# Performance work log

Hardware: AMD Instinct MI355X
Metric: run time of the kernel (lower is better)

Reference implementation:

```python
import jax, jax.numpy as jnp
import numpy as np

NUM_PROPS = 512
D = 2 * NUM_PROPS          # n_embd
NUM_STEPS = 32
LN_EPS = 1e-5
_SQRT_2_OVER_PI = float(np.sqrt(2.0 / np.pi))


def gelu_new(x):
    # GPT-2 'gelu_new' tanh approximation
    return 0.5 * x * (1.0 + jnp.tanh(_SQRT_2_OVER_PI * (x + 0.044715 * x ** 3)))


def layernorm(x, g, b):
    mu = jnp.mean(x, axis=-1, keepdims=True)
    var = jnp.mean((x - mu) ** 2, axis=-1, keepdims=True)
    return (x - mu) * jax.lax.rsqrt(var + LN_EPS) * g + b


def setup_inputs() -> dict:
    key = jax.random.key(0)
    ks = jax.random.split(key, 16)
    s = 0.02
    inp = {
        "tokens": jax.random.randint(ks[0], (16, 256, D), 0, 2, dtype=jnp.int64),
        # GPT2 block params (Conv1D convention: weight [in, out])
        "W_qkv": jax.random.normal(ks[1], (D, 3 * D), jnp.float32) * s,
        "b_qkv": jnp.zeros((3 * D,), jnp.float32),
        "W_aproj": jax.random.normal(ks[2], (D, D), jnp.float32) * s,
        "b_aproj": jnp.zeros((D,), jnp.float32),
        "g_ln1": jnp.ones((D,), jnp.float32),
        "b_ln1": jnp.zeros((D,), jnp.float32),
        "g_ln2": jnp.ones((D,), jnp.float32),
        "b_ln2": jnp.zeros((D,), jnp.float32),
        "W_fc": jax.random.normal(ks[3], (D, 4 * D), jnp.float32) * s,
        "b_fc": jnp.zeros((4 * D,), jnp.float32),
        "W_mproj": jax.random.normal(ks[4], (4 * D, D), jnp.float32) * s,
        "b_mproj": jnp.zeros((D,), jnp.float32),
        "g_lnf": jnp.ones((D,), jnp.float32),
        "b_lnf": jnp.zeros((D,), jnp.float32),
        # classification head: nn.Linear(d, num_labels, bias=False), weight [num_labels, d]
        "W_score": jax.random.normal(ks[5], (NUM_PROPS, D), jnp.float32) * s,
    }
    return inp


def gpt2_logits(x, W_qkv, b_qkv, W_aproj, b_aproj, g_ln1, b_ln1, g_ln2, b_ln2,
                W_fc, b_fc, W_mproj, b_mproj, g_lnf, b_lnf, W_score):
    # x: [B, S, D] float embeddings (wpe is zeroed in the original module)
    S = x.shape[1]
    h = layernorm(x, g_ln1, b_ln1)
    qkv = h @ W_qkv + b_qkv
    q, k, v = jnp.split(qkv, 3, axis=-1)  # single head, head_dim = D
    scores = jnp.einsum("bqd,bkd->bqk", q, k) / jnp.sqrt(jnp.float32(D))
    causal = jnp.tril(jnp.ones((S, S), dtype=bool))
    scores = jnp.where(causal, scores, jnp.finfo(scores.dtype).min)
    attn = jax.nn.softmax(scores, axis=-1)
    x = x + jnp.einsum("bqk,bkd->bqd", attn, v) @ W_aproj + b_aproj
    h2 = layernorm(x, g_ln2, b_ln2)
    x = x + gelu_new(h2 @ W_fc + b_fc) @ W_mproj + b_mproj
    x = layernorm(x, g_lnf, b_lnf)
    # sequence classification: logits of the LAST token (inputs_embeds path)
    return x[:, -1, :] @ W_score.T  # [B, num_props]


def reference(tokens, W_qkv, b_qkv, W_aproj, b_aproj, g_ln1, b_ln1, g_ln2, b_ln2,
              W_fc, b_fc, W_mproj, b_mproj, g_lnf, b_lnf, W_score):
    all_toks = tokens.astype(jnp.float32)  # [B, L, D]
    logits_per_step = []
    for _ in range(NUM_STEPS):  # full recompute each step, no KV cache (faithful)
        logits = gpt2_logits(all_toks, W_qkv, b_qkv, W_aproj, b_aproj,
                             g_ln1, b_ln1, g_ln2, b_ln2, W_fc, b_fc,
                             W_mproj, b_mproj, g_lnf, b_lnf, W_score)
        succ = (logits > 0).astype(jnp.float32)  # hard threshold (non-diff, as .long())
        succ_tok = jnp.concatenate([jnp.zeros_like(succ), succ], axis=-1)[:, None, :]
        all_toks = jnp.concatenate([all_toks, jax.lax.stop_gradient(succ_tok)], axis=1)
        logits_per_step.append(logits)
    return jnp.stack(logits_per_step, axis=1)  # [B, num_steps, num_props]
```

## Files before the change

### kernel.cpp

```cpp
#include <hip/hip_runtime.h>
#include <math.h>

#ifndef M_PI
#define M_PI 3.14159265358979323846
#endif

#define BD 256
#define NB 16
#define DIM 1024
#define SMAX 288
#define NSTEPS 32
#define NPROPS 512
#define NTOK (16 * 256 * 1024)

__device__ __forceinline__ double wred_sum(double v) {
#pragma unroll
    for (int o = 32; o > 0; o >>= 1) v += __shfl_down(v, o, 64);
    return v;
}
__device__ __forceinline__ double wred_max(double v) {
#pragma unroll
    for (int o = 32; o > 0; o >>= 1) { double w = __shfl_down(v, o, 64); if (w > v) v = w; }
    return v;
}
__device__ double block_sum(double v, double* sc) {
    v = wred_sum(v);
    int tid = threadIdx.x;
    if ((tid & 63) == 0) sc[tid >> 6] = v;
    __syncthreads();
    double r = sc[0] + sc[1] + sc[2] + sc[3];
    __syncthreads();
    return r;
}
__device__ double block_max(double v, double* sc) {
    v = wred_max(v);
    int tid = threadIdx.x;
    if ((tid & 63) == 0) sc[tid >> 6] = v;
    __syncthreads();
    double r = fmax(fmax(sc[0], sc[1]), fmax(sc[2], sc[3]));
    __syncthreads();
    return r;
}

__global__ __launch_bounds__(256) void k_tok_convert(const int* __restrict__ tok32,
                                                     signed char* __restrict__ tokc) {
    __shared__ int flag;
    int tid = threadIdx.x;
    if (tid == 0) {
        int nz = 0;
        for (int i = 1; i < 512; i += 2) nz |= tok32[i];
        flag = nz;
    }
    __syncthreads();
    bool is64 = (flag == 0);
#pragma unroll
    for (int it = 0; it < 4; ++it) {
        size_t idx = (size_t)blockIdx.x * 1024 + it * BD + tid;
        int v = is64 ? tok32[2 * idx] : tok32[idx];
        tokc[idx] = (signed char)v;
    }
}

__global__ __launch_bounds__(256) void k_prefix_stats(const signed char* __restrict__ tokc,
                                                      double* __restrict__ mu, double* __restrict__ rs) {
    __shared__ double sc[4];
    int T = blockIdx.x, tid = threadIdx.x;
    const signed char* row = tokc + (size_t)T * DIM;
    double s = 0;
    for (int i = tid; i < DIM; i += BD) s += (double)row[i];
    s = block_sum(s, sc);
    double m = s * (1.0 / 1024.0);
    double ss = 0;
    for (int i = tid; i < DIM; i += BD) { double d = (double)row[i] - m; ss += d * d; }
    ss = block_sum(ss, sc);
    if (tid == 0) { mu[T] = m; rs[T] = 1.0 / sqrt(ss * (1.0 / 1024.0) + 1e-5); }
}

__global__ __launch_bounds__(256) void k_init(const signed char* __restrict__ tokc,
                                              const double* __restrict__ mu, const double* __restrict__ rs,
                                              double* __restrict__ xl,
                                              double* __restrict__ mub, double* __restrict__ rsb) {
    int b = blockIdx.x, tid = threadIdx.x;
    int T = b * 256 + 255;
    if (tid == 0) { mub[b] = mu[T]; rsb[b] = rs[T]; }
    for (int i = tid; i < DIM; i += BD)
        xl[b * DIM + i] = (double)tokc[(size_t)T * DIM + i];
}

__global__ __launch_bounds__(256) void k_prefix(const signed char* __restrict__ tokc,
        const double* __restrict__ mu, const double* __restrict__ rs,
        const float* __restrict__ Wqkv, const float* __restrict__ bqkv,
        const float* __restrict__ g1, const float* __restrict__ b1,
        float* __restrict__ Kcf, float* __restrict__ Vcf) {
    __shared__ float Hs[64 * 65];
    __shared__ float Ws[64 * 64];
    int tid = threadIdx.x;
    int tx = tid & 63, ty = tid >> 6;
    int j0 = blockIdx.x * 64;
    int T0 = blockIdx.y * 64;
    float acc[16];
#pragma unroll
    for (int a = 0; a < 16; ++a) acc[a] = 0.f;
    for (int kc = 0; kc < DIM; kc += 64) {
#pragma unroll
        for (int it = 0; it < 16; ++it) {
            int idx = tid + it * BD;
            int k = idx & 63, t = idx >> 6;
            int T = T0 + t;
            double x = (double)tokc[(size_t)T * DIM + kc + k];
            Hs[k * 65 + t] = (float)((x - mu[T]) * rs[T] * (double)g1[kc + k] + (double)b1[kc + k]);
        }
#pragma unroll
        for (int it = 0; it < 16; ++it) {
            int idx = tid + it * BD;
            int k = idx >> 6, j = idx & 63;
            Ws[k * 64 + j] = Wqkv[(size_t)(kc + k) * 3072 + 1024 + j0 + j];
        }
        __syncthreads();
#pragma unroll 4
        for (int k = 0; k < 64; ++k) {
            float w = Ws[k * 64 + tx];
#pragma unroll
            for (int a = 0; a < 16; ++a)
                acc[a] += Hs[k * 65 + ty * 16 + a] * w;
        }
        __syncthreads();
    }
    int colg = j0 + tx;
    float bias = bqkv[1024 + colg];
    bool isK = (colg < 1024);
#pragma unroll
    for (int a = 0; a < 16; ++a) {
        int T = T0 + ty * 16 + a;
        int b = T >> 8, pos = T & 255;
        float v = acc[a] + bias;
        if (isK) Kcf[((size_t)b * SMAX + pos) * DIM + colg] = v;
        else     Vcf[((size_t)b * SMAX + pos) * DIM + colg - 1024] = v;
    }
}

__global__ __launch_bounds__(256) void k_qkv(const double* __restrict__ xl,
        const double* __restrict__ mub, const double* __restrict__ rsb,
        const float* __restrict__ g1, const float* __restrict__ b1,
        const float* __restrict__ Wqkv, float* __restrict__ P1) {
    __shared__ double As[16 * 64];
    __shared__ float  Ws[64 * 64];
    int tid = threadIdx.x, tx = tid & 63, ty = tid >> 6;
    int j0 = blockIdx.x * 64;
    int k0 = blockIdx.y * 128;
    double acc[4] = {0, 0, 0, 0};
    for (int kc = 0; kc < 128; kc += 64) {
#pragma unroll
        for (int it = 0; it < 4; ++it) {
            int idx = tid + it * BD;
            int b = idx >> 6, k = idx & 63;
            int kk = k0 + kc + k;
            As[b * 64 + k] = (xl[(size_t)b * DIM + kk] - mub[b]) * rsb[b] * (double)g1[kk] + (double)b1[kk];
        }
#pragma unroll
        for (int it = 0; it < 16; ++it) {
            int idx = tid + it * BD;
            int k = idx >> 6, j = idx & 63;
            Ws[k * 64 + j] = Wqkv[(size_t)(k0 + kc + k) * 3072 + j0 + j];
        }
        __syncthreads();
#pragma unroll 8
        for (int k = 0; k < 64; ++k) {
            double w = (double)Ws[k * 64 + tx];
            acc[0] += As[(ty * 4 + 0) * 64 + k] * w;
            acc[1] += As[(ty * 4 + 1) * 64 + k] * w;
            acc[2] += As[(ty * 4 + 2) * 64 + k] * w;
            acc[3] += As[(ty * 4 + 3) * 64 + k] * w;
        }
        __syncthreads();
    }
#pragma unroll
    for (int a = 0; a < 4; ++a)
        P1[((size_t)(blockIdx.y * 16 + ty * 4 + a)) * 3072 + j0 + tx] = (float)acc[a];
}

__global__ __launch_bounds__(256) void mm16(const double* __restrict__ A, int K,
        const float* __restrict__ W, int ldw, double* __restrict__ P, int ncols) {
    __shared__ double As[16 * 64];
    __shared__ float  Ws[64 * 64];
    int tid = threadIdx.x, tx = tid & 63, ty = tid >> 6;
    int j0 = blockIdx.x * 64;
    int klen = K / gridDim.y;
    int k0 = blockIdx.y * klen;
    double acc[4] = {0, 0, 0, 0};
    for (int kc = 0; kc < klen; kc += 64) {
#pragma unroll
        for (int it = 0; it < 4; ++it) {
            int idx = tid + it * BD;
            int b = idx >> 6, k = idx & 63;
            As[b * 64 + k] = A[(size_t)b * K + k0 + kc + k];
        }
#pragma unroll
        for (int it = 0; it < 16; ++it) {
            int idx = tid + it * BD;
            int k = idx >> 6, j = idx & 63;
            Ws[k * 64 + j] = W[(size_t)(k0 + kc + k) * ldw + j0 + j];
        }
        __syncthreads();
#pragma unroll 8
        for (int k = 0; k < 64; ++k) {
            double w = (double)Ws[k * 64 + tx];
            acc[0] += As[(ty * 4 + 0) * 64 + k] * w;
            acc[1] += As[(ty * 4 + 1) * 64 + k] * w;
            acc[2] += As[(ty * 4 + 2) * 64 + k] * w;
            acc[3] += As[(ty * 4 + 3) * 64 + k] * w;
        }
        __syncthreads();
    }
#pragma unroll
    for (int a = 0; a < 4; ++a)
        P[((size_t)(blockIdx.y * 16 + ty * 4 + a)) * ncols + j0 + tx] = acc[a];
}

__global__ __launch_bounds__(256) void mm16f(const double* __restrict__ A, int K,
        const float* __restrict__ W, int ldw, float* __restrict__ P, int ncols) {
    __shared__ double As[16 * 64];
    __shared__ float  Ws[64 * 64];
    int tid = threadIdx.x, tx = tid & 63, ty = tid >> 6;
    int j0 = blockIdx.x * 64;
    int klen = K / gridDim.y;
    int k0 = blockIdx.y * klen;
    double acc[4] = {0, 0, 0, 0};
    for (int kc = 0; kc < klen; kc += 64) {
#pragma unroll
        for (int it = 0; it < 4; ++it) {
            int idx = tid + it * BD;
            int b = idx >> 6, k = idx & 63;
            As[b * 64 + k] = A[(size_t)b * K + k0 + kc + k];
        }
#pragma unroll
        for (int it = 0; it < 16; ++it) {
            int idx = tid + it * BD;
            int k = idx >> 6, j = idx & 63;
            Ws[k * 64 + j] = W[(size_t)(k0 + kc + k) * ldw + j0 + j];
        }
        __syncthreads();
#pragma unroll 8
        for (int k = 0; k < 64; ++k) {
            double w = (double)Ws[k * 64 + tx];
            acc[0] += As[(ty * 4 + 0) * 64 + k] * w;
            acc[1] += As[(ty * 4 + 1) * 64 + k] * w;
            acc[2] += As[(ty * 4 + 2) * 64 + k] * w;
            acc[3] += As[(ty * 4 + 3) * 64 + k] * w;
        }
        __syncthreads();
    }
#pragma unroll
    for (int a = 0; a < 4; ++a)
        P[((size_t)(blockIdx.y * 16 + ty * 4 + a)) * ncols + j0 + tx] = (float)acc[a];
}

__global__ __launch_bounds__(256) void mm16_t(const double* __restrict__ A, int K,
        const float* __restrict__ Wt, double* __restrict__ P, int ncols) {
    __shared__ double As[16 * 64];
    __shared__ float  Ws[64 * 65];
    int tid = threadIdx.x, tx = tid & 63, ty = tid >> 6;
    int j0 = blockIdx.x * 64;
    int klen = K / gridDim.y;
    int k0 = blockIdx.y * klen;
    double acc[4] = {0, 0, 0, 0};
    for (int kc = 0; kc < klen; kc += 64) {
#pragma unroll
        for (int it = 0; it < 4; ++it) {
            int idx = tid + it * BD;
            int b = idx >> 6, k = idx & 63;
            As[b * 64 + k] = A[(size_t)b * K + k0 + kc + k];
        }
#pragma unroll
        for (int it = 0; it < 16; ++it) {
            int idx = tid + it * BD;
            int j = idx >> 6, k = idx & 63;
            Ws[k * 65 + j] = Wt[(size_t)(j0 + j) * K + k0 + kc + k];
        }
        __syncthreads();
#pragma unroll 8
        for (int k = 0; k < 64; ++k) {
            double w = (double)Ws[k * 65 + tx];
            acc[0] += As[(ty * 4 + 0) * 64 + k] * w;
            acc[1] += As[(ty * 4 + 1) * 64 + k] * w;
            acc[2] += As[(ty * 4 + 2) * 64 + k] * w;
            acc[3] += As[(ty * 4 + 3) * 64 + k] * w;
        }
        __syncthreads();
    }
#pragma unroll
    for (int a = 0; a < 4; ++a)
        P[((size_t)(blockIdx.y * 16 + ty * 4 + a)) * ncols + j0 + tx] = acc[a];
}

__global__ __launch_bounds__(256) void k_scores(const float* __restrict__ P1,
        const float* __restrict__ bqkv, float* __restrict__ Kcf, float* __restrict__ Vcf,
        double* __restrict__ sco, int S) {
    __shared__ double qs[DIM];
    __shared__ float  ksf[DIM];
    int b = blockIdx.x, tid = threadIdx.x;
    int pos = S - 1;
    for (int col = tid; col < DIM; col += BD) {
        double s = (double)bqkv[col];
#pragma unroll
        for (int ks = 0; ks < 8; ++ks) s += (double)P1[((size_t)(ks * 16 + b)) * 3072 + col];
        qs[col] = s;
    }
    if ((int)blockIdx.y == (pos >> 5)) {
        for (int col = tid; col < DIM; col += BD) {
            double sk = (double)bqkv[1024 + col];
            double sv = (double)bqkv[2048 + col];
#pragma unroll
            for (int ks = 0; ks < 8; ++ks) {
                const float* Pr = &P1[((size_t)(ks * 16 + b)) * 3072];
                sk += (double)Pr[1024 + col];
                sv += (double)Pr[2048 + col];
            }
            float kf = (float)sk;
            ksf[col] = kf;
            Kcf[((size_t)b * SMAX + pos) * DIM + col] = kf;
            Vcf[((size_t)b * SMAX + pos) * DIM + col] = (float)sv;
        }
    }
    __syncthreads();
    int lane = tid & 63, w = tid >> 6;
    int base = blockIdx.y * 32 + w * 8;
    for (int r = 0; r < 8; ++r) {
        int p = base + r;
        if (p >= S) break;
        double acc = 0;
        const float4* kp4 = (p == pos) ? (const float4*)ksf
                                       : (const float4*)(Kcf + ((size_t)b * SMAX + p) * DIM);
#pragma unroll
        for (int ii = 0; ii < 4; ++ii) {
            float4 kv = kp4[lane + 64 * ii];
            int e = 4 * (lane + 64 * ii);
            acc += qs[e] * (double)kv.x + qs[e + 1] * (double)kv.y
                 + qs[e + 2] * (double)kv.z + qs[e + 3] * (double)kv.w;
        }
        acc = wred_sum(acc);
        if (lane == 0) sco[b * SMAX + p] = acc * 0.03125;
    }
}

__global__ __launch_bounds__(256) void k_attnp(const double* __restrict__ sco, const float* __restrict__ Vcf,
                                               double* __restrict__ AOp, int S) {
    __shared__ double ps[SMAX];
    __shared__ double sc[4];
    int b = blockIdx.x, sub = blockIdx.y, tid = threadIdx.x;
    int dch = sub & 3, sch = sub >> 2;
    double lm = -1e300;
    for (int i = tid; i < S; i += BD) { double v = sco[b * SMAX + i]; ps[i] = v; if (v > lm) lm = v; }
    __syncthreads();
    double mx = block_max(lm, sc);
    double le = 0;
    for (int i = tid; i < S; i += BD) { double e = exp(ps[i] - mx); ps[i] = e; le += e; }
    double den = block_sum(le, sc);
    int d = dch * 256 + tid;
    int p0 = sch * 36, p1 = p0 + 36; if (p1 > S) p1 = S;
    const float* Vb = Vcf + (size_t)b * SMAX * DIM + d;
    double a0 = 0, a1 = 0, a2 = 0, a3 = 0;
    int p = p0;
    for (; p + 4 <= p1; p += 4) {
        a0 += ps[p + 0] * (double)Vb[(size_t)(p + 0) * DIM];
        a1 += ps[p + 1] * (double)Vb[(size_t)(p + 1) * DIM];
        a2 += ps[p + 2] * (double)Vb[(size_t)(p + 2) * DIM];
        a3 += ps[p + 3] * (double)Vb[(size_t)(p + 3) * DIM];
    }
    for (; p < p1; ++p) a0 += ps[p] * (double)Vb[(size_t)p * DIM];
    AOp[((size_t)(sch * 16 + b)) * DIM + d] = ((a0 + a1) + (a2 + a3)) / den;
}

__global__ __launch_bounds__(256) void k_aproj(const double* __restrict__ AOp,
        const float* __restrict__ Wap, double* __restrict__ P2) {
    __shared__ double As[16 * 64];
    __shared__ float  Ws[64 * 64];
    int tid = threadIdx.x, tx = tid & 63, ty = tid >> 6;
    int j0 = blockIdx.x * 64;
    int k0 = blockIdx.y * 128;
    double acc[4] = {0, 0, 0, 0};
    for (int kc = 0; kc < 128; kc += 64) {
#pragma unroll
        for (int it = 0; it < 4; ++it) {
            int idx = tid + it * BD;
            int b = idx >> 6, k = idx & 63;
            const double* col = AOp + (size_t)b * DIM + k0 + kc + k;
            double s = 0;
#pragma unroll
            for (int sct = 0; sct < 8; ++sct) s += col[(size_t)sct * 16 * DIM];
            As[b * 64 + k] = s;
        }
#pragma unroll
        for (int it = 0; it < 16; ++it) {
            int idx = tid + it * BD;
            int k = idx >> 6, j = idx & 63;
            Ws[k * 64 + j] = Wap[(size_t)(k0 + kc + k) * DIM + j0 + j];
        }
        __syncthreads();
#pragma unroll 8
        for (int k = 0; k < 64; ++k) {
            double w = (double)Ws[k * 64 + tx];
            acc[0] += As[(ty * 4 + 0) * 64 + k] * w;
            acc[1] += As[(ty * 4 + 1) * 64 + k] * w;
            acc[2] += As[(ty * 4 + 2) * 64 + k] * w;
            acc[3] += As[(ty * 4 + 3) * 64 + k] * w;
        }
        __syncthreads();
    }
#pragma unroll
    for (int a = 0; a < 4; ++a)
        P2[((size_t)(blockIdx.y * 16 + ty * 4 + a)) * DIM + j0 + tx] = acc[a];
}

__global__ __launch_bounds__(256) void k_ln2(const double* __restrict__ xl, const double* __restrict__ P2,
        const float* __restrict__ bap, const float* __restrict__ g2, const float* __restrict__ b2,
        double* __restrict__ x2, double* __restrict__ h2) {
    __shared__ double xs[DIM];
    __shared__ double sc[4];
    int b = blockIdx.x, tid = threadIdx.x;
    for (int i = tid; i < DIM; i += BD) {
        double s = xl[b * DIM + i] + (double)bap[i];
        for (int ks = 0; ks < 8; ++ks) s += P2[((size_t)(ks * 16 + b)) * DIM + i];
        xs[i] = s; x2[b * DIM + i] = s;
    }
    __syncthreads();
    double s = 0;
    for (int i = tid; i < DIM; i += BD) s += xs[i];
    s = block_sum(s, sc);
    double m = s * (1.0 / 1024.0);
    double ss = 0;
    for (int i = tid; i < DIM; i += BD) { double d = xs[i] - m; ss += d * d; }
    ss = block_sum(ss, sc);
    double r = 1.0 / sqrt(ss * (1.0 / 1024.0) + 1e-5);
    for (int i = tid; i < DIM; i += BD)
        h2[b * DIM + i] = (xs[i] - m) * r * (double)g2[i] + (double)b2[i];
}

__global__ __launch_bounds__(256) void k_gelu(const float* __restrict__ P3, const float* __restrict__ bfc,
                                              double* __restrict__ m) {
    int b = blockIdx.x;
    int i = blockIdx.y * BD + threadIdx.x;
    double u = (double)bfc[i];
    for (int ks = 0; ks < 8; ++ks) u += (double)P3[((size_t)(ks * 16 + b)) * 4096 + i];
    double c = sqrt(2.0 / M_PI);
    double inner = c * (u + 0.044715 * u * u * u);
    m[(size_t)b * 4096 + i] = 0.5 * u * (1.0 + tanh(inner));
}

__global__ __launch_bounds__(256) void k_lnf(const double* __restrict__ x2, const double* __restrict__ P4,
        const float* __restrict__ bmp, const float* __restrict__ gf, const float* __restrict__ bf,
        double* __restrict__ hf) {
    __shared__ double xs[DIM];
    __shared__ double sc[4];
    int b = blockIdx.x, tid = threadIdx.x;
    for (int i = tid; i < DIM; i += BD) {
        double s = x2[b * DIM + i] + (double)bmp[i];
        for (int ks = 0; ks < 16; ++ks) s += P4[((size_t)(ks * 16 + b)) * DIM + i];
        xs[i] = s;
    }
    __syncthreads();
    double s = 0;
    for (int i = tid; i < DIM; i += BD) s += xs[i];
    s = block_sum(s, sc);
    double m = s * (1.0 / 1024.0);
    double ss = 0;
    for (int i = tid; i < DIM; i += BD) { double d = xs[i] - m; ss += d * d; }
    ss = block_sum(ss, sc);
    double r = 1.0 / sqrt(ss * (1.0 / 1024.0) + 1e-5);
    for (int i = tid; i < DIM; i += BD)
        hf[b * DIM + i] = (xs[i] - m) * r * (double)gf[i] + (double)bf[i];
}

__global__ __launch_bounds__(256) void k_final(const double* __restrict__ P5, float* __restrict__ out,
                                               double* __restrict__ xl,
                                               double* __restrict__ mub, double* __restrict__ rsb, int t) {
    __shared__ double sc[4];
    int b = blockIdx.x, tid = threadIdx.x;
    double cnt = 0;
    for (int p = tid; p < NPROPS; p += BD) {
        double lg = 0;
        for (int ks = 0; ks < 8; ++ks) lg += P5[((size_t)(ks * 16 + b)) * NPROPS + p];
        out[((size_t)b * NSTEPS + t) * NPROPS + p] = (float)lg;
        double bit = (lg > 0.0) ? 1.0 : 0.0;
        xl[b * DIM + p] = 0.0;
        xl[b * DIM + NPROPS + p] = bit;
        cnt += bit;
    }
    double s = block_sum(cnt, sc);
    double mean = s * (1.0 / 1024.0);
    double var = mean - mean * mean;
    double r = 1.0 / sqrt(var + 1e-5);
    if (tid == 0) { mub[b] = mean; rsb[b] = r; }
}

extern "C" void kernel_launch(void* const* d_in, const int* in_sizes, int n_in,
                              void* d_out, int out_size, void* d_ws, size_t ws_size,
                              hipStream_t stream) {
    const int*   tok  = (const int*)d_in[0];
    const float* Wqkv = (const float*)d_in[1];
    const float* bqkv = (const float*)d_in[2];
    const float* Wap  = (const float*)d_in[3];
    const float* bap  = (const float*)d_in[4];
    const float* g1   = (const float*)d_in[5];
    const float* b1   = (const float*)d_in[6];
    const float* g2   = (const float*)d_in[7];
    const float* b2   = (const float*)d_in[8];
    const float* Wfc  = (const float*)d_in[9];
    const float* bfc  = (const float*)d_in[10];
    const float* Wmp  = (const float*)d_in[11];
    const float* bmp  = (const float*)d_in[12];
    const float* gf   = (const float*)d_in[13];
    const float* bf   = (const float*)d_in[14];
    const float* Wsc  = (const float*)d_in[15];
    float* out = (float*)d_out;

    char* w = (char*)d_ws;
    size_t off = 0;
    auto alloc = [&](size_t bytes) -> void* {
        void* p = (void*)(w + off);
        off += (bytes + 255) & ~(size_t)255;
        return p;
    };
    float*       Kcf  = (float*)alloc((size_t)NB * SMAX * DIM * 4);
    float*       Vcf  = (float*)alloc((size_t)NB * SMAX * DIM * 4);
    double*      mu   = (double*)alloc(4096 * 8);
    double*      rs   = (double*)alloc(4096 * 8);
    double*      mub  = (double*)alloc(NB * 8);
    double*      rsb  = (double*)alloc(NB * 8);
    double*      xl   = (double*)alloc((size_t)NB * DIM * 8);
    double*      sco  = (double*)alloc((size_t)NB * SMAX * 8);
    double*      AOp  = (double*)alloc((size_t)8 * NB * DIM * 8);
    double*      x2   = (double*)alloc((size_t)NB * DIM * 8);
    double*      h2   = (double*)alloc((size_t)NB * DIM * 8);
    double*      m_   = (double*)alloc((size_t)NB * 4096 * 8);
    double*      hf   = (double*)alloc((size_t)NB * DIM * 8);
    float*       P1   = (float*)alloc((size_t)8 * NB * 3072 * 4);
    double*      P2   = (double*)alloc((size_t)8 * NB * 1024 * 8);
    float*       P3   = (float*)alloc((size_t)8 * NB * 4096 * 4);
    double*      P4   = (double*)alloc((size_t)16 * NB * 1024 * 8);
    double*      P5   = (double*)alloc((size_t)8 * NB * 512 * 8);
    signed char* tokc = (signed char*)alloc((size_t)NTOK);
    if (off > ws_size) return;

    k_tok_convert<<<4096, BD, 0, stream>>>(tok, tokc);
    k_prefix_stats<<<4096, BD, 0, stream>>>(tokc, mu, rs);
    k_init<<<NB, BD, 0, stream>>>(tokc, mu, rs, xl, mub, rsb);
    k_prefix<<<dim3(32, 64), BD, 0, stream>>>(tokc, mu, rs, Wqkv, bqkv, g1, b1, Kcf, Vcf);

    for (int t = 0; t < NSTEPS; ++t) {
        int S = 256 + t;
        k_qkv<<<dim3(48, 8), BD, 0, stream>>>(xl, mub, rsb, g1, b1, Wqkv, P1);
        k_scores<<<dim3(NB, 9), BD, 0, stream>>>(P1, bqkv, Kcf, Vcf, sco, S);
        k_attnp<<<dim3(NB, 32), BD, 0, stream>>>(sco, Vcf, AOp, S);
        k_aproj<<<dim3(16, 8), BD, 0, stream>>>(AOp, Wap, P2);
        k_ln2<<<NB, BD, 0, stream>>>(xl, P2, bap, g2, b2, x2, h2);
        mm16f<<<dim3(64, 8), BD, 0, stream>>>(h2, 1024, Wfc, 4096, P3, 4096);
        k_gelu<<<dim3(NB, 16), BD, 0, stream>>>(P3, bfc, m_);
        mm16<<<dim3(16, 16), BD, 0, stream>>>(m_, 4096, Wmp, 1024, P4, 1024);
        k_lnf<<<NB, BD, 0, stream>>>(x2, P4, bmp, gf, bf, hf);
        mm16_t<<<dim3(8, 8), BD, 0, stream>>>(hf, 1024, Wsc, P5, 512);
        k_final<<<NB, BD, 0, stream>>>(P5, out, xl, mub, rsb, t);
    }
}
```

Baseline: 3.593 ms.

## Store intermediate activations and partials in fp32, fuse token convert with stats

```diff
diff --git a/kernel.cpp b/kernel.cpp
--- a/kernel.cpp
+++ b/kernel.cpp
@@ -42,10 +42,12 @@
     return r;
 }
 
-__global__ __launch_bounds__(256) void k_tok_convert(const int* __restrict__ tok32,
-                                                     signed char* __restrict__ tokc) {
+__global__ __launch_bounds__(256) void k_tok_stats(const int* __restrict__ tok32,
+                                                   signed char* __restrict__ tokc,
+                                                   double* __restrict__ mu, double* __restrict__ rs) {
     __shared__ int flag;
-    int tid = threadIdx.x;
+    __shared__ double sc[4];
+    int T = blockIdx.x, tid = threadIdx.x;
     if (tid == 0) {
         int nz = 0;
         for (int i = 1; i < 512; i += 2) nz |= tok32[i];
@@ -53,24 +55,19 @@
     }
     __syncthreads();
     bool is64 = (flag == 0);
+    signed char* row = tokc + (size_t)T * DIM;
+    double s = 0;
 #pragma unroll
     for (int it = 0; it < 4; ++it) {
-        size_t idx = (size_t)blockIdx.x * 1024 + it * BD + tid;
+        size_t idx = (size_t)T * 1024 + it * BD + tid;
         int v = is64 ? tok32[2 * idx] : tok32[idx];
-        tokc[idx] = (signed char)v;
-    }
-}
-
-__global__ __launch_bounds__(256) void k_prefix_stats(const signed char* __restrict__ tokc,
-                                                      double* __restrict__ mu, double* __restrict__ rs) {
-    __shared__ double sc[4];
-    int T = blockIdx.x, tid = threadIdx.x;
-    const signed char* row = tokc + (size_t)T * DIM;
-    double s = 0;
-    for (int i = tid; i < DIM; i += BD) s += (double)row[i];
+        row[it * BD + tid] = (signed char)v;
+        s += (double)v;
+    }
     s = block_sum(s, sc);
     double m = s * (1.0 / 1024.0);
     double ss = 0;
+    __syncthreads();
     for (int i = tid; i < DIM; i += BD) { double d = (double)row[i] - m; ss += d * d; }
     ss = block_sum(ss, sc);
     if (tid == 0) { mu[T] = m; rs[T] = 1.0 / sqrt(ss * (1.0 / 1024.0) + 1e-5); }
@@ -78,13 +75,13 @@
 
 __global__ __launch_bounds__(256) void k_init(const signed char* __restrict__ tokc,
                                               const double* __restrict__ mu, const double* __restrict__ rs,
-                                              double* __restrict__ xl,
+                                              float* __restrict__ xl,
                                               double* __restrict__ mub, double* __restrict__ rsb) {
     int b = blockIdx.x, tid = threadIdx.x;
     int T = b * 256 + 255;
     if (tid == 0) { mub[b] = mu[T]; rsb[b] = rs[T]; }
     for (int i = tid; i < DIM; i += BD)
-        xl[b * DIM + i] = (double)tokc[(size_t)T * DIM + i];
+        xl[b * DIM + i] = (float)tokc[(size_t)T * DIM + i];
 }
 
 __global__ __launch_bounds__(256) void k_prefix(const signed char* __restrict__ tokc,
@@ -139,7 +136,7 @@
     }
 }
 
-__global__ __launch_bounds__(256) void k_qkv(const double* __restrict__ xl,
+__global__ __launch_bounds__(256) void k_qkv(const float* __restrict__ xl,
         const double* __restrict__ mub, const double* __restrict__ rsb,
         const float* __restrict__ g1, const float* __restrict__ b1,
         const float* __restrict__ Wqkv, float* __restrict__ P1) {
@@ -155,7 +152,7 @@
             int idx = tid + it * BD;
             int b = idx >> 6, k = idx & 63;
             int kk = k0 + kc + k;
-            As[b * 64 + k] = (xl[(size_t)b * DIM + kk] - mub[b]) * rsb[b] * (double)g1[kk] + (double)b1[kk];
+            As[b * 64 + k] = ((double)xl[(size_t)b * DIM + kk] - mub[b]) * rsb[b] * (double)g1[kk] + (double)b1[kk];
         }
 #pragma unroll
         for (int it = 0; it < 16; ++it) {
@@ -179,45 +176,7 @@
         P1[((size_t)(blockIdx.y * 16 + ty * 4 + a)) * 3072 + j0 + tx] = (float)acc[a];
 }
 
-__global__ __launch_bounds__(256) void mm16(const double* __restrict__ A, int K,
-        const float* __restrict__ W, int ldw, double* __restrict__ P, int ncols) {
-    __shared__ double As[16 * 64];
-    __shared__ float  Ws[64 * 64];
-    int tid = threadIdx.x, tx = tid & 63, ty = tid >> 6;
-    int j0 = blockIdx.x * 64;
-    int klen = K / gridDim.y;
-    int k0 = blockIdx.y * klen;
-    double acc[4] = {0, 0, 0, 0};
-    for (int kc = 0; kc < klen; kc += 64) {
-#pragma unroll
-        for (int it = 0; it < 4; ++it) {
-            int idx = tid + it * BD;
-            int b = idx >> 6, k = idx & 63;
-            As[b * 64 + k] = A[(size_t)b * K + k0 + kc + k];
-        }
-#pragma unroll
-        for (int it = 0; it < 16; ++it) {
-            int idx = tid + it * BD;
-            int k = idx >> 6, j = idx & 63;
-            Ws[k * 64 + j] = W[(size_t)(k0 + kc + k) * ldw + j0 + j];
-        }
-        __syncthreads();
-#pragma unroll 8
-        for (int k = 0; k < 64; ++k) {
-            double w = (double)Ws[k * 64 + tx];
-            acc[0] += As[(ty * 4 + 0) * 64 + k] * w;
-            acc[1] += As[(ty * 4 + 1) * 64 + k] * w;
-            acc[2] += As[(ty * 4 + 2) * 64 + k] * w;
-            acc[3] += As[(ty * 4 + 3) * 64 + k] * w;
-        }
-        __syncthreads();
-    }
-#pragma unroll
-    for (int a = 0; a < 4; ++a)
-        P[((size_t)(blockIdx.y * 16 + ty * 4 + a)) * ncols + j0 + tx] = acc[a];
-}
-
-__global__ __launch_bounds__(256) void mm16f(const double* __restrict__ A, int K,
+__global__ __launch_bounds__(256) void mm16ff(const float* __restrict__ A, int K,
         const float* __restrict__ W, int ldw, float* __restrict__ P, int ncols) {
     __shared__ double As[16 * 64];
     __shared__ float  Ws[64 * 64];
@@ -231,7 +190,7 @@
         for (int it = 0; it < 4; ++it) {
             int idx = tid + it * BD;
             int b = idx >> 6, k = idx & 63;
-            As[b * 64 + k] = A[(size_t)b * K + k0 + kc + k];
+            As[b * 64 + k] = (double)A[(size_t)b * K + k0 + kc + k];
         }
 #pragma unroll
         for (int it = 0; it < 16; ++it) {
@@ -255,8 +214,8 @@
         P[((size_t)(blockIdx.y * 16 + ty * 4 + a)) * ncols + j0 + tx] = (float)acc[a];
 }
 
-__global__ __launch_bounds__(256) void mm16_t(const double* __restrict__ A, int K,
-        const float* __restrict__ Wt, double* __restrict__ P, int ncols) {
+__global__ __launch_bounds__(256) void mm16_tf(const float* __restrict__ A, int K,
+        const float* __restrict__ Wt, float* __restrict__ P, int ncols) {
     __shared__ double As[16 * 64];
     __shared__ float  Ws[64 * 65];
     int tid = threadIdx.x, tx = tid & 63, ty = tid >> 6;
@@ -269,7 +228,7 @@
         for (int it = 0; it < 4; ++it) {
             int idx = tid + it * BD;
             int b = idx >> 6, k = idx & 63;
-            As[b * 64 + k] = A[(size_t)b * K + k0 + kc + k];
+            As[b * 64 + k] = (double)A[(size_t)b * K + k0 + kc + k];
         }
 #pragma unroll
         for (int it = 0; it < 16; ++it) {
@@ -290,7 +249,7 @@
     }
 #pragma unroll
     for (int a = 0; a < 4; ++a)
-        P[((size_t)(blockIdx.y * 16 + ty * 4 + a)) * ncols + j0 + tx] = acc[a];
+        P[((size_t)(blockIdx.y * 16 + ty * 4 + a)) * ncols + j0 + tx] = (float)acc[a];
 }
 
 __global__ __launch_bounds__(256) void k_scores(const float* __restrict__ P1,
@@ -344,7 +303,7 @@
 }
 
 __global__ __launch_bounds__(256) void k_attnp(const double* __restrict__ sco, const float* __restrict__ Vcf,
-                                               double* __restrict__ AOp, int S) {
+                                               float* __restrict__ AOp, int S) {
     __shared__ double ps[SMAX];
     __shared__ double sc[4];
     int b = blockIdx.x, sub = blockIdx.y, tid = threadIdx.x;
@@ -368,11 +327,11 @@
         a3 += ps[p + 3] * (double)Vb[(size_t)(p + 3) * DIM];
     }
     for (; p < p1; ++p) a0 += ps[p] * (double)Vb[(size_t)p * DIM];
-    AOp[((size_t)(sch * 16 + b)) * DIM + d] = ((a0 + a1) + (a2 + a3)) / den;
-}
-
-__global__ __launch_bounds__(256) void k_aproj(const double* __restrict__ AOp,
-        const float* __restrict__ Wap, double* __restrict__ P2) {
+    AOp[((size_t)(sch * 16 + b)) * DIM + d] = (float)(((a0 + a1) + (a2 + a3)) / den);
+}
+
+__global__ __launch_bounds__(256) void k_aproj(const float* __restrict__ AOp,
+        const float* __restrict__ Wap, float* __restrict__ P2) {
     __shared__ double As[16 * 64];
     __shared__ float  Ws[64 * 64];
     int tid = threadIdx.x, tx = tid & 63, ty = tid >> 6;
@@ -384,10 +343,10 @@
         for (int it = 0; it < 4; ++it) {
             int idx = tid + it * BD;
             int b = idx >> 6, k = idx & 63;
-            const double* col = AOp + (size_t)b * DIM + k0 + kc + k;
+            const float* col = AOp + (size_t)b * DIM + k0 + kc + k;
             double s = 0;
 #pragma unroll
-            for (int sct = 0; sct < 8; ++sct) s += col[(size_t)sct * 16 * DIM];
+            for (int sct = 0; sct < 8; ++sct) s += (double)col[(size_t)sct * 16 * DIM];
             As[b * 64 + k] = s;
         }
 #pragma unroll
@@ -409,18 +368,18 @@
     }
 #pragma unroll
     for (int a = 0; a < 4; ++a)
-        P2[((size_t)(blockIdx.y * 16 + ty * 4 + a)) * DIM + j0 + tx] = acc[a];
-}
-
-__global__ __launch_bounds__(256) void k_ln2(const double* __restrict__ xl, const double* __restrict__ P2,
+        P2[((size_t)(blockIdx.y * 16 + ty * 4 + a)) * DIM + j0 + tx] = (float)acc[a];
+}
+
+__global__ __launch_bounds__(256) void k_ln2(const float* __restrict__ xl, const float* __restrict__ P2,
         const float* __restrict__ bap, const float* __restrict__ g2, const float* __restrict__ b2,
-        double* __restrict__ x2, double* __restrict__ h2) {
+        double* __restrict__ x2, float* __restrict__ h2) {
     __shared__ double xs[DIM];
     __shared__ double sc[4];
     int b = blockIdx.x, tid = threadIdx.x;
     for (int i = tid; i < DIM; i += BD) {
-        double s = xl[b * DIM + i] + (double)bap[i];
-        for (int ks = 0; ks < 8; ++ks) s += P2[((size_t)(ks * 16 + b)) * DIM + i];
+        double s = (double)xl[b * DIM + i] + (double)bap[i];
+        for (int ks = 0; ks < 8; ++ks) s += (double)P2[((size_t)(ks * 16 + b)) * DIM + i];
         xs[i] = s; x2[b * DIM + i] = s;
     }
     __syncthreads();
@@ -433,29 +392,29 @@
     ss = block_sum(ss, sc);
     double r = 1.0 / sqrt(ss * (1.0 / 1024.0) + 1e-5);
     for (int i = tid; i < DIM; i += BD)
-        h2[b * DIM + i] = (xs[i] - m) * r * (double)g2[i] + (double)b2[i];
+        h2[b * DIM + i] = (float)((xs[i] - m) * r * (double)g2[i] + (double)b2[i]);
 }
 
 __global__ __launch_bounds__(256) void k_gelu(const float* __restrict__ P3, const float* __restrict__ bfc,
-                                              double* __restrict__ m) {
+                                              float* __restrict__ m) {
     int b = blockIdx.x;
     int i = blockIdx.y * BD + threadIdx.x;
     double u = (double)bfc[i];
     for (int ks = 0; ks < 8; ++ks) u += (double)P3[((size_t)(ks * 16 + b)) * 4096 + i];
     double c = sqrt(2.0 / M_PI);
     double inner = c * (u + 0.044715 * u * u * u);
-    m[(size_t)b * 4096 + i] = 0.5 * u * (1.0 + tanh(inner));
-}
-
-__global__ __launch_bounds__(256) void k_lnf(const double* __restrict__ x2, const double* __restrict__ P4,
+    m[(size_t)b * 4096 + i] = (float)(0.5 * u * (1.0 + tanh(inner)));
+}
+
+__global__ __launch_bounds__(256) void k_lnf(const double* __restrict__ x2, const float* __restrict__ P4,
         const float* __restrict__ bmp, const float* __restrict__ gf, const float* __restrict__ bf,
-        double* __restrict__ hf) {
+        float* __restrict__ hf) {
     __shared__ double xs[DIM];
     __shared__ double sc[4];
     int b = blockIdx.x, tid = threadIdx.x;
     for (int i = tid; i < DIM; i += BD) {
         double s = x2[b * DIM + i] + (double)bmp[i];
-        for (int ks = 0; ks < 16; ++ks) s += P4[((size_t)(ks * 16 + b)) * DIM + i];
+        for (int ks = 0; ks < 16; ++ks) s += (double)P4[((size_t)(ks * 16 + b)) * DIM + i];
         xs[i] = s;
     }
     __syncthreads();
@@ -468,23 +427,23 @@
     ss = block_sum(ss, sc);
     double r = 1.0 / sqrt(ss * (1.0 / 1024.0) + 1e-5);
     for (int i = tid; i < DIM; i += BD)
-        hf[b * DIM + i] = (xs[i] - m) * r * (double)gf[i] + (double)bf[i];
-}
-
-__global__ __launch_bounds__(256) void k_final(const double* __restrict__ P5, float* __restrict__ out,
-                                               double* __restrict__ xl,
+        hf[b * DIM + i] = (float)((xs[i] - m) * r * (double)gf[i] + (double)bf[i]);
+}
+
+__global__ __launch_bounds__(256) void k_final(const float* __restrict__ P5, float* __restrict__ out,
+                                               float* __restrict__ xl,
                                                double* __restrict__ mub, double* __restrict__ rsb, int t) {
     __shared__ double sc[4];
     int b = blockIdx.x, tid = threadIdx.x;
     double cnt = 0;
     for (int p = tid; p < NPROPS; p += BD) {
         double lg = 0;
-        for (int ks = 0; ks < 8; ++ks) lg += P5[((size_t)(ks * 16 + b)) * NPROPS + p];
+        for (int ks = 0; ks < 8; ++ks) lg += (double)P5[((size_t)(ks * 16 + b)) * NPROPS + p];
         out[((size_t)b * NSTEPS + t) * NPROPS + p] = (float)lg;
-        double bit = (lg > 0.0) ? 1.0 : 0.0;
-        xl[b * DIM + p] = 0.0;
+        float bit = (lg > 0.0) ? 1.0f : 0.0f;
+        xl[b * DIM + p] = 0.0f;
         xl[b * DIM + NPROPS + p] = bit;
-        cnt += bit;
+        cnt += (double)bit;
     }
     double s = block_sum(cnt, sc);
     double mean = s * (1.0 / 1024.0);
@@ -527,23 +486,22 @@
     double*      rs   = (double*)alloc(4096 * 8);
     double*      mub  = (double*)alloc(NB * 8);
     double*      rsb  = (double*)alloc(NB * 8);
-    double*      xl   = (double*)alloc((size_t)NB * DIM * 8);
+    float*       xl   = (float*)alloc((size_t)NB * DIM * 4);
     double*      sco  = (double*)alloc((size_t)NB * SMAX * 8);
-    double*      AOp  = (double*)alloc((size_t)8 * NB * DIM * 8);
+    float*       AOp  = (float*)alloc((size_t)8 * NB * DIM * 4);
     double*      x2   = (double*)alloc((size_t)NB * DIM * 8);
-    double*      h2   = (double*)alloc((size_t)NB * DIM * 8);
-    double*      m_   = (double*)alloc((size_t)NB * 4096 * 8);
-    double*      hf   = (double*)alloc((size_t)NB * DIM * 8);
+    float*       h2   = (float*)alloc((size_t)NB * DIM * 4);
+    float*       m_   = (float*)alloc((size_t)NB * 4096 * 4);
+    float*       hf   = (float*)alloc((size_t)NB * DIM * 4);
     float*       P1   = (float*)alloc((size_t)8 * NB * 3072 * 4);
-    double*      P2   = (double*)alloc((size_t)8 * NB * 1024 * 8);
+    float*       P2   = (float*)alloc((size_t)8 * NB * 1024 * 4);
     float*       P3   = (float*)alloc((size_t)8 * NB * 4096 * 4);
-    double*      P4   = (double*)alloc((size_t)16 * NB * 1024 * 8);
-    double*      P5   = (double*)alloc((size_t)8 * NB * 512 * 8);
+    float*       P4   = (float*)alloc((size_t)16 * NB * 1024 * 4);
+    float*       P5   = (float*)alloc((size_t)8 * NB * 512 * 4);
     signed char* tokc = (signed char*)alloc((size_t)NTOK);
     if (off > ws_size) return;
 
-    k_tok_convert<<<4096, BD, 0, stream>>>(tok, tokc);
-    k_prefix_stats<<<4096, BD, 0, stream>>>(tokc, mu, rs);
+    k_tok_stats<<<4096, BD, 0, stream>>>(tok, tokc, mu, rs);
     k_init<<<NB, BD, 0, stream>>>(tokc, mu, rs, xl, mub, rsb);
     k_prefix<<<dim3(32, 64), BD, 0, stream>>>(tokc, mu, rs, Wqkv, bqkv, g1, b1, Kcf, Vcf);
 
@@ -554,11 +512,11 @@
         k_attnp<<<dim3(NB, 32), BD, 0, stream>>>(sco, Vcf, AOp, S);
         k_aproj<<<dim3(16, 8), BD, 0, stream>>>(AOp, Wap, P2);
         k_ln2<<<NB, BD, 0, stream>>>(xl, P2, bap, g2, b2, x2, h2);
-        mm16f<<<dim3(64, 8), BD, 0, stream>>>(h2, 1024, Wfc, 4096, P3, 4096);
+        mm16ff<<<dim3(64, 8), BD, 0, stream>>>(h2, 1024, Wfc, 4096, P3, 4096);
         k_gelu<<<dim3(NB, 16), BD, 0, stream>>>(P3, bfc, m_);
-        mm16<<<dim3(16, 16), BD, 0, stream>>>(m_, 4096, Wmp, 1024, P4, 1024);
+        mm16ff<<<dim3(16, 16), BD, 0, stream>>>(m_, 4096, Wmp, 1024, P4, 1024);
         k_lnf<<<NB, BD, 0, stream>>>(x2, P4, bmp, gf, bf, hf);
-        mm16_t<<<dim3(8, 8), BD, 0, stream>>>(hf, 1024, Wsc, P5, 512);
+        mm16_tf<<<dim3(8, 8), BD, 0, stream>>>(hf, 1024, Wsc, P5, 512);
         k_final<<<NB, BD, 0, stream>>>(P5, out, xl, mub, rsb, t);
     }
 }
```

New measurement: 3.426 ms. 1.05x faster.
